# Performance work log

Hardware: AMD Instinct MI355X
Metric: run time of the kernel (lower is better)

Reference implementation:

```python
import jax, jax.numpy as jnp
import numpy as np

N, E, D, G = 50000, 640000, 128, 64
STEPS = 4

def _leaky(z):
    return jnp.where(z >= 0, z, 0.01 * z)

def _lin(x, W, b):
    return x @ W.T + b

def setup_inputs() -> dict:
    key = jax.random.key(0)
    ks = jax.random.split(key, 16)
    s = 0.05
    inp = {
        "x": jax.random.normal(ks[0], (N, D), jnp.float32),
        "x_global": jax.random.normal(ks[1], (G, D), jnp.float32),
        "edge_attr": jax.random.normal(ks[2], (E, 2), jnp.float32),
        # per-step stacked parameters (torch Linear layout [out,in])
        "Wm": jax.random.normal(ks[3], (STEPS, D, D), jnp.float32) * s,
        "bm": jnp.zeros((STEPS, D), jnp.float32),
        "Wa": jax.random.normal(ks[4], (STEPS, D, 2 * D), jnp.float32) * s,
        "ba": jnp.zeros((STEPS, D), jnp.float32),
        "Wgate": jax.random.normal(ks[5], (STEPS, 1, D), jnp.float32) * s,
        "bgate": jnp.zeros((STEPS, 1), jnp.float32),
        "Wfeat": jax.random.normal(ks[6], (STEPS, D, D), jnp.float32) * s,
        "bfeat": jnp.zeros((STEPS, D), jnp.float32),
        "Wt": jax.random.normal(ks[7], (STEPS, D, 2 * D), jnp.float32) * s,
        "bt": jnp.zeros((STEPS, D), jnp.float32),
        "edge_index": jax.random.randint(ks[8], (2, E), 0, N, jnp.int32),
        "batch_ind": jnp.sort(jax.random.randint(ks[9], (N,), 0, G, jnp.int32)),
        "num_graphs": G,
    }
    return inp

def reference(x, x_global, edge_attr, Wm, bm, Wa, ba, Wgate, bgate, Wfeat, bfeat, Wt, bt, edge_index, batch_ind, num_graphs):
    src, dst = edge_index[0], edge_index[1]
    n = x.shape[0]
    for i in range(Wm.shape[0]):
        # GraphNet: gather -> Linear+LeakyReLU -> scatter-max -> concat -> Linear+LeakyReLU + residual
        msg = _leaky(_lin(x[src], Wm[i], bm[i]))                     # [E, agg]
        agg = jax.ops.segment_max(msg, dst, num_segments=n)
        agg = jnp.where(jnp.isfinite(agg), agg, 0.0)                 # PyG fills empty with 0
        x = _leaky(_lin(jnp.concatenate([x, agg], axis=1), Wa[i], ba[i])) + x
        # GlobalNode: attentional aggregation (segment softmax) + transform + residual
        gate = _lin(x, Wgate[i], bgate[i])[:, 0]                     # [N]
        feat = _leaky(_lin(x, Wfeat[i], bfeat[i]))                   # [N, D]
        gmax = jax.ops.segment_max(gate, batch_ind, num_segments=num_graphs)
        gmax = jnp.where(jnp.isfinite(gmax), gmax, 0.0)
        e = jnp.exp(gate - gmax[batch_ind])
        denom = jax.ops.segment_sum(e, batch_ind, num_segments=num_graphs)
        denom = jnp.where(denom == 0, 1.0, denom)
        alpha = e / denom[batch_ind]
        xg = jax.ops.segment_sum(alpha[:, None] * feat, batch_ind, num_segments=num_graphs)
        cat = jnp.concatenate([xg, x_global], axis=1)
        x_global = _leaky(_lin(cat, Wt[i], bt[i])) + x_global
    return (x, x_global)
```

## Files before the change

### kernel.cpp

```cpp
#include <hip/hip_runtime.h>
#include <hip/hip_bf16.h>

#define NN 50000
#define EE 640000
#define DD 128
#define GG 64
#define STEPS 4
#define XP 32
#define NB 196

static inline int cdiv(int a, int b) { return (a + b - 1) / b; }

typedef __attribute__((ext_vector_type(8))) short bf16x8;
typedef __attribute__((ext_vector_type(4))) float f32x4;

__device__ __forceinline__ float lk(float z) { return z >= 0.f ? z : 0.01f * z; }
__device__ __forceinline__ float b2f(short b) { return __uint_as_float(((unsigned)(unsigned short)b) << 16); }
__device__ __forceinline__ unsigned short f2b(float f) {
    unsigned u = __float_as_uint(f);
    return (unsigned short)((u + 0x7FFFu + ((u >> 16) & 1u)) >> 16);
}

__global__ void k_f2b(const float* __restrict__ in, unsigned short* __restrict__ out, int n4) {
    int i = blockIdx.x * blockDim.x + threadIdx.x;
    if (i < n4) {
        float4 v = reinterpret_cast<const float4*>(in)[i];
        ushort4 o;
        o.x = f2b(v.x); o.y = f2b(v.y); o.z = f2b(v.z); o.w = f2b(v.w);
        reinterpret_cast<ushort4*>(out)[i] = o;
    }
}

#define WC1 (STEPS * DD * DD / 4)
#define WC2 (STEPS * DD * 2 * DD / 4)
#define WC3 (STEPS * DD * DD / 4)
__global__ void k_wcvt(const float* __restrict__ Wm, const float* __restrict__ Wa, const float* __restrict__ Wf,
                       unsigned short* __restrict__ Wm_b, unsigned short* __restrict__ Wa_b,
                       unsigned short* __restrict__ Wf_b) {
    int i = blockIdx.x * blockDim.x + threadIdx.x;
    const float* src; unsigned short* dst; int j = i;
    if (j < WC1) { src = Wm; dst = Wm_b; }
    else {
        j -= WC1;
        if (j < WC2) { src = Wa; dst = Wa_b; }
        else {
            j -= WC2;
            if (j >= WC3) return;
            src = Wf; dst = Wf_b;
        }
    }
    float4 v = reinterpret_cast<const float4*>(src)[j];
    ushort4 o;
    o.x = f2b(v.x); o.y = f2b(v.y); o.z = f2b(v.z); o.w = f2b(v.w);
    reinterpret_cast<ushort4*>(dst)[j] = o;
}

__global__ void k_count(const int* __restrict__ dst, int* __restrict__ deg) {
    int e = blockIdx.x * blockDim.x + threadIdx.x;
    if (e < EE) atomicAdd(&deg[dst[e]], 1);
}

__global__ __launch_bounds__(256) void k_scan1(const int* __restrict__ deg, int* __restrict__ off,
                                               int* __restrict__ bsum) {
    __shared__ int ws[4];
    int tid = threadIdx.x, lane = tid & 63, wv = tid >> 6;
    int i = blockIdx.x * 256 + tid;
    int v = (i < NN) ? deg[i] : 0;
    int x = v;
    #pragma unroll
    for (int o = 1; o < 64; o <<= 1) { int t = __shfl_up(x, o); if (lane >= o) x += t; }
    if (lane == 63) ws[wv] = x;
    __syncthreads();
    int wbase = 0;
    #pragma unroll
    for (int p = 0; p < 3; ++p) if (p < wv) wbase += ws[p];
    if (i < NN) off[i] = wbase + x - v;
    if (tid == 255) bsum[blockIdx.x] = wbase + x;
}

__global__ __launch_bounds__(256) void k_scan2(const int* __restrict__ bsum, int* __restrict__ boff,
                                               int* __restrict__ off) {
    __shared__ int ws[4];
    int tid = threadIdx.x, lane = tid & 63, wv = tid >> 6;
    int v = (tid < NB) ? bsum[tid] : 0;
    int x = v;
    #pragma unroll
    for (int o = 1; o < 64; o <<= 1) { int t = __shfl_up(x, o); if (lane >= o) x += t; }
    if (lane == 63) ws[wv] = x;
    __syncthreads();
    int wbase = 0;
    #pragma unroll
    for (int p = 0; p < 3; ++p) if (p < wv) wbase += ws[p];
    if (tid < NB) boff[tid] = wbase + x - v;
    if (tid == 255) off[NN] = wbase + x;
}

__global__ __launch_bounds__(256) void k_scan3(const int* __restrict__ boff, int* __restrict__ off,
                                               int* __restrict__ cursor) {
    int i = blockIdx.x * 256 + threadIdx.x;
    if (i < NN) {
        int o = off[i] + boff[blockIdx.x];
        off[i] = o;
        cursor[i] = o;
    }
}

__global__ void k_fill(const int* __restrict__ src, const int* __restrict__ dst,
                       int* __restrict__ cursor, int* __restrict__ csr) {
    int e = blockIdx.x * blockDim.x + threadIdx.x;
    if (e < EE) {
        int d = dst[e];
        int p = atomicAdd(&cursor[d], 1);
        csr[p] = src[e];
    }
}

__global__ void k_goff(const int* __restrict__ batch, int* __restrict__ goff) {
    int i = blockIdx.x * blockDim.x + threadIdx.x;
    if (i >= NN) return;
    int b = batch[i];
    int prev = (i == 0) ? -1 : batch[i - 1];
    for (int g = prev + 1; g <= b; ++g) goff[g] = i;
    if (i == NN - 1) for (int g = b + 1; g <= GG; ++g) goff[g] = NN;
}

template<int KDIM, bool TWO_IN, bool RESID, bool GATE, bool OUT2>
__global__ __launch_bounds__(256) void k_mfma(
    const unsigned short* __restrict__ X1b, const unsigned short* __restrict__ X2b,
    const unsigned short* __restrict__ W1, const float* __restrict__ b1,
    const unsigned short* __restrict__ W2, const float* __restrict__ b2,
    unsigned short* __restrict__ Yb1, unsigned short* __restrict__ Yb2,
    float* __restrict__ Yf, const float* __restrict__ resid,
    const float* __restrict__ wgf, const float* __restrict__ bgp, float* __restrict__ efac)
{
    __shared__ float sY[32 * 128];
    const int tid = threadIdx.x;
    const int wv = tid >> 6, lane = tid & 63;
    const int lo = lane & 15, hi = lane >> 4;
    const int rw = wv >> 1, cw = wv & 1;
    const int n0 = blockIdx.x * 32;
    const int arow = n0 + rw * 16 + lo;
    const bool rvalid = arow < NN;

    constexpr int KCH = KDIM / 32;

    bf16x8 a[KCH];
    #pragma unroll
    for (int kc = 0; kc < KCH; ++kc) {
        const int k = kc * 32 + hi * 8;
        if (rvalid) {
            if (TWO_IN) {
                const unsigned short* base = (kc < 4) ? &X1b[(size_t)arow * 128 + k]
                                                      : &X2b[(size_t)arow * 128 + (k - 128)];
                a[kc] = *reinterpret_cast<const bf16x8*>(base);
            } else {
                a[kc] = *reinterpret_cast<const bf16x8*>(&X1b[(size_t)arow * KDIM + k]);
            }
        } else {
            a[kc] = (bf16x8)(short)0;
        }
    }

    f32x4 acc1[4], acc2[4];
    #pragma unroll
    for (int t = 0; t < 4; ++t) { acc1[t] = (f32x4){0.f,0.f,0.f,0.f}; acc2[t] = (f32x4){0.f,0.f,0.f,0.f}; }

    #pragma unroll
    for (int kc = 0; kc < KCH; ++kc) {
        const int k = kc * 32 + hi * 8;
        #pragma unroll
        for (int t = 0; t < 4; ++t) {
            const int o = cw * 64 + t * 16 + lo;
            bf16x8 bv = *reinterpret_cast<const bf16x8*>(&W1[(size_t)o * KDIM + k]);
            acc1[t] = __builtin_amdgcn_mfma_f32_16x16x32_bf16(a[kc], bv, acc1[t], 0, 0, 0);
            if (OUT2) {
                bf16x8 bv2 = *reinterpret_cast<const bf16x8*>(&W2[(size_t)o * KDIM + k]);
                acc2[t] = __builtin_amdgcn_mfma_f32_16x16x32_bf16(a[kc], bv2, acc2[t], 0, 0, 0);
            }
        }
    }

    const int lrow = rw * 16 + hi * 4;
    const int swz = (hi & 1) << 4;
    #pragma unroll
    for (int t = 0; t < 4; ++t) {
        const int oc = cw * 64 + t * 16 + lo;
        const int col = oc ^ swz;
        const float bc = b1[oc];
        #pragma unroll
        for (int r = 0; r < 4; ++r)
            sY[(lrow + r) * 128 + col] = lk(acc1[t][r] + bc);
    }
    __syncthreads();

    if (RESID) {
        const float bg0 = GATE ? bgp[0] : 0.f;
        #pragma unroll
        for (int it = 0; it < 4; ++it) {
            const int idx = it * 256 + tid;
            const int row = idx >> 5, u4 = (idx & 31) * 4;
            const int n = n0 + row;
            const bool valid = n < NN;
            const int ux = u4 ^ (((row >> 2) & 1) << 4);
            float4 v = *reinterpret_cast<const float4*>(&sY[row * 128 + ux]);
            if (valid) {
                float4 rsd = *reinterpret_cast<const float4*>(&resid[(size_t)n * 128 + u4]);
                v.x += rsd.x; v.y += rsd.y; v.z += rsd.z; v.w += rsd.w;
                *reinterpret_cast<float4*>(&Yf[(size_t)n * 128 + u4]) = v;
                ushort4 ob;
                ob.x = f2b(v.x); ob.y = f2b(v.y); ob.z = f2b(v.z); ob.w = f2b(v.w);
                *reinterpret_cast<ushort4*>(&Yb1[(size_t)n * 128 + u4]) = ob;
            }
            if (GATE) {
                float4 wg4 = *reinterpret_cast<const float4*>(&wgf[u4]);
                float gs = valid ? (v.x * wg4.x + v.y * wg4.y + v.z * wg4.z + v.w * wg4.w) : 0.f;
                #pragma unroll
                for (int sh = 16; sh > 0; sh >>= 1) gs += __shfl_xor(gs, sh);
                if ((lane & 31) == 0 && valid) efac[n] = __expf(gs + bg0);
            }
        }
    } else {
        #pragma unroll
        for (int it = 0; it < 2; ++it) {
            const int idx = it * 256 + tid;
            const int row = idx >> 4, ub = (idx & 15) * 8;
            const int n = n0 + row;
            if (n < NN) {
                const int ubx = ub ^ (((row >> 2) & 1) << 4);
                bf16x8 ob;
                #pragma unroll
                for (int j = 0; j < 8; ++j) ob[j] = (short)f2b(sY[row * 128 + ubx + j]);
                *reinterpret_cast<bf16x8*>(&Yb1[(size_t)n * 128 + ub]) = ob;
            }
        }
    }

    if (OUT2) {
        __syncthreads();
        #pragma unroll
        for (int t = 0; t < 4; ++t) {
            const int oc = cw * 64 + t * 16 + lo;
            const int col = oc ^ swz;
            const float bc = b2[oc];
            #pragma unroll
            for (int r = 0; r < 4; ++r)
                sY[(lrow + r) * 128 + col] = lk(acc2[t][r] + bc);
        }
        __syncthreads();
        #pragma unroll
        for (int it = 0; it < 2; ++it) {
            const int idx = it * 256 + tid;
            const int row = idx >> 4, ub = (idx & 15) * 8;
            const int n = n0 + row;
            if (n < NN) {
                const int ubx = ub ^ (((row >> 2) & 1) << 4);
                bf16x8 ob;
                #pragma unroll
                for (int j = 0; j < 8; ++j) ob[j] = (short)f2b(sY[row * 128 + ubx + j]);
                *reinterpret_cast<bf16x8*>(&Yb2[(size_t)n * 128 + ub]) = ob;
            }
        }
    }
}

__global__ __launch_bounds__(256) void k_aggmax(const unsigned short* __restrict__ yb,
                                                const int* __restrict__ off,
                                                const int* __restrict__ csr,
                                                unsigned short* __restrict__ aggb) {
    int gtid = blockIdx.x * blockDim.x + threadIdx.x;
    int node = gtid >> 6;
    if (node >= NN) return;
    int lane = threadIdx.x & 63;
    int slot = lane >> 4, c8 = (lane & 15) * 8;
    int b = off[node], e = off[node + 1];
    int deg = e - b;
    float m[8];
    #pragma unroll
    for (int j = 0; j < 8; ++j) m[j] = -3.4e38f;
    if (deg > 0) {
        int T = (deg + 7) >> 3;
        for (int it = 0; it < T; ++it) {
            int p0 = b + it * 8 + slot;
            int p1 = p0 + 4;
            int i0 = csr[p0 < e ? p0 : b];
            int i1 = csr[p1 < e ? p1 : b];
            bf16x8 v0 = *reinterpret_cast<const bf16x8*>(&yb[(size_t)i0 * 128 + c8]);
            bf16x8 v1 = *reinterpret_cast<const bf16x8*>(&yb[(size_t)i1 * 128 + c8]);
            #pragma unroll
            for (int j = 0; j < 8; ++j) m[j] = fmaxf(m[j], fmaxf(b2f(v0[j]), b2f(v1[j])));
        }
    }
    #pragma unroll
    for (int j = 0; j < 8; ++j) m[j] = fmaxf(m[j], __shfl_xor(m[j], 16));
    #pragma unroll
    for (int j = 0; j < 8; ++j) m[j] = fmaxf(m[j], __shfl_xor(m[j], 32));
    if (slot == 0) {
        bf16x8 o;
        #pragma unroll
        for (int j = 0; j < 8; ++j) o[j] = (deg > 0) ? (short)f2b(m[j]) : (short)0;
        *reinterpret_cast<bf16x8*>(&aggb[(size_t)node * 128 + c8]) = o;
    }
}

__global__ __launch_bounds__(128) void k_xgpart(const float* __restrict__ efac,
                                                const unsigned short* __restrict__ featb,
                                                const int* __restrict__ goff,
                                                float* __restrict__ part, float* __restrict__ parte) {
    int g = blockIdx.x >> 5, p = blockIdx.x & 31;
    int d = threadIdx.x;
    int b = goff[g], e = goff[g + 1];
    int len = e - b;
    int chunk = (len + XP - 1) / XP;
    int s0 = b + p * chunk;
    int s1 = min(e, s0 + chunk);
    float acc = 0.f, acce = 0.f;
    #pragma unroll 2
    for (int i = s0; i < s1; ++i) {
        float ev = efac[i];
        acce += ev;
        acc += ev * b2f(featb[(size_t)i * 128 + d]);
    }
    part[((size_t)g * XP + p) * 128 + d] = acc;
    if (d == 0) parte[(size_t)g * XP + p] = acce;
}

__global__ __launch_bounds__(128) void k_gtrans(const float* __restrict__ part, const float* __restrict__ parte,
                                                const float* __restrict__ Wt, const float* __restrict__ bt,
                                                float* __restrict__ xglob) {
    __shared__ float cat[256];
    int g = blockIdx.x;
    int o = threadIdx.x;
    float xgv = 0.f, se = 0.f;
    #pragma unroll
    for (int p = 0; p < XP; ++p) {
        xgv += part[((size_t)g * XP + p) * 128 + o];
        se  += parte[(size_t)g * XP + p];
    }
    if (se == 0.f) se = 1.f;
    cat[o] = xgv / se;
    cat[128 + o] = xglob[(size_t)g * 128 + o];
    __syncthreads();
    float accv = bt[o];
    const float4* w4 = reinterpret_cast<const float4*>(&Wt[(size_t)o * 256]);
    #pragma unroll 8
    for (int k4 = 0; k4 < 64; ++k4) {
        float4 wv = w4[k4];
        accv += cat[4 * k4 + 0] * wv.x + cat[4 * k4 + 1] * wv.y + cat[4 * k4 + 2] * wv.z + cat[4 * k4 + 3] * wv.w;
    }
    float outv = lk(accv) + cat[128 + o];
    xglob[(size_t)g * 128 + o] = outv;
}

extern "C" void kernel_launch(void* const* d_in, const int* in_sizes, int n_in,
                              void* d_out, int out_size, void* d_ws, size_t ws_size,
                              hipStream_t stream) {
    const float* x_in  = (const float*)d_in[0];
    const float* xg_in = (const float*)d_in[1];
    const float* Wm = (const float*)d_in[3];
    const float* bm = (const float*)d_in[4];
    const float* Wa = (const float*)d_in[5];
    const float* ba = (const float*)d_in[6];
    const float* Wg = (const float*)d_in[7];
    const float* bg = (const float*)d_in[8];
    const float* Wf = (const float*)d_in[9];
    const float* bf = (const float*)d_in[10];
    const float* Wt = (const float*)d_in[11];
    const float* bt = (const float*)d_in[12];
    const int* eidx  = (const int*)d_in[13];
    const int* batch = (const int*)d_in[14];

    float* xout  = (float*)d_out;
    float* xglob = xout + (size_t)NN * DD;

    char* w = (char*)d_ws;
    unsigned short* yb    = (unsigned short*)w; w += (size_t)NN * DD * 2;
    unsigned short* featb = (unsigned short*)w; w += (size_t)NN * DD * 2;
    unsigned short* aggb  = (unsigned short*)w; w += (size_t)NN * DD * 2;
    unsigned short* xb    = (unsigned short*)w; w += (size_t)NN * DD * 2;
    unsigned short* Wm_b  = (unsigned short*)w; w += (size_t)STEPS * DD * DD * 2;
    unsigned short* Wa_b  = (unsigned short*)w; w += (size_t)STEPS * DD * 2 * DD * 2;
    unsigned short* Wf_b  = (unsigned short*)w; w += (size_t)STEPS * DD * DD * 2;
    float* efac   = (float*)w; w += (size_t)NN * 4;
    float* part   = (float*)w; w += (size_t)GG * XP * DD * 4;
    float* parte  = (float*)w; w += (size_t)GG * XP * 4;
    int* deg    = (int*)w; w += (size_t)(NN + 1) * 4;
    int* off    = (int*)w; w += (size_t)(NN + 1) * 4;
    int* cursor = (int*)w; w += (size_t)NN * 4;
    int* csr    = (int*)w; w += (size_t)EE * 4;
    int* goff   = (int*)w; w += (size_t)(GG + 1) * 4;
    int* bsum   = (int*)w; w += (size_t)NB * 4;
    int* boff   = (int*)w; w += (size_t)NB * 4;

    const int* srcI = eidx;
    const int* dstI = eidx + EE;

    hipMemcpyAsync(xout,  x_in,  (size_t)NN * DD * 4, hipMemcpyDeviceToDevice, stream);
    hipMemcpyAsync(xglob, xg_in, (size_t)GG * DD * 4, hipMemcpyDeviceToDevice, stream);

    k_f2b<<<cdiv(NN * DD / 4, 256), 256, 0, stream>>>(x_in, xb, NN * DD / 4);
    k_wcvt<<<cdiv(WC1 + WC2 + WC3, 256), 256, 0, stream>>>(Wm, Wa, Wf, Wm_b, Wa_b, Wf_b);

    hipMemsetAsync(deg, 0, (size_t)NN * 4, stream);
    k_count<<<cdiv(EE, 256), 256, 0, stream>>>(dstI, deg);
    k_scan1<<<NB, 256, 0, stream>>>(deg, off, bsum);
    k_scan2<<<1, 256, 0, stream>>>(bsum, boff, off);
    k_scan3<<<NB, 256, 0, stream>>>(boff, off, cursor);
    k_fill<<<cdiv(EE, 256), 256, 0, stream>>>(srcI, dstI, cursor, csr);
    k_goff<<<cdiv(NN, 256), 256, 0, stream>>>(batch, goff);

    const int gemmGrid = cdiv(NN, 32);
    const int aggGrid  = cdiv(NN * 64, 256);

    k_mfma<128, false, false, false, false><<<gemmGrid, 256, 0, stream>>>(
        xb, nullptr, Wm_b, bm, nullptr, nullptr, yb, nullptr, nullptr, nullptr, nullptr, nullptr, nullptr);

    for (int i = 0; i < STEPS; ++i) {
        const float* bai = ba + (size_t)i * DD;
        const unsigned short* Wai = Wa_b + (size_t)i * DD * 2 * DD;
        const float* Wgi = Wg + (size_t)i * DD;
        const float* bgi = bg + (size_t)i;
        const unsigned short* Wfi = Wf_b + (size_t)i * DD * DD;
        const float* bfi = bf + (size_t)i * DD;
        const float* Wti = Wt + (size_t)i * DD * 2 * DD;
        const float* bti = bt + (size_t)i * DD;

        k_aggmax<<<aggGrid, 256, 0, stream>>>(yb, off, csr, aggb);
        k_mfma<256, true, true, true, false><<<gemmGrid, 256, 0, stream>>>(
            xb, aggb, Wai, bai, nullptr, nullptr, xb, nullptr, xout, xout, Wgi, bgi, efac);
        if (i < STEPS - 1) {
            const unsigned short* Wmn = Wm_b + (size_t)(i + 1) * DD * DD;
            const float* bmn = bm + (size_t)(i + 1) * DD;
            k_mfma<128, false, false, false, true><<<gemmGrid, 256, 0, stream>>>(
                xb, nullptr, Wfi, bfi, Wmn, bmn, featb, yb, nullptr, nullptr, nullptr, nullptr, nullptr);
        } else {
            k_mfma<128, false, false, false, false><<<gemmGrid, 256, 0, stream>>>(
                xb, nullptr, Wfi, bfi, nullptr, nullptr, featb, nullptr, nullptr, nullptr, nullptr, nullptr, nullptr);
        }
        k_xgpart<<<GG * XP, 128, 0, stream>>>(efac, featb, goff, part, parte);
        k_gtrans<<<GG, 128, 0, stream>>>(part, parte, Wti, bti, xglob);
    }
}
```

Measured before the change: 556.2 us.

## Fuse aggregation GEMM with feature/message GEMMs into one kernel per step

Merges the Wa GEMM (with residual, gate and exp) and the following Wfeat/Wm GEMMs into a single kernel. The updated bf16 x tile stays in shared memory and feeds the second GEMM directly, so the x re-read and one launch per step go away. It also drops the initial fp32 copy of x by reading the residual from x_in on step 0, and doubles the graph-partition count in the global pooling kernel with deeper unrolling. The trade-off is more shared memory and registers per block, which may lower occupancy.

```diff
diff --git a/kernel.cpp b/kernel.cpp
--- a/kernel.cpp
+++ b/kernel.cpp
@@ -6,7 +6,7 @@
 #define DD 128
 #define GG 64
 #define STEPS 4
-#define XP 32
+#define XP 64
 #define NB 196
 
 static inline int cdiv(int a, int b) { return (a + b - 1) / b; }
@@ -124,14 +124,9 @@
     if (i == NN - 1) for (int g = b + 1; g <= GG; ++g) goff[g] = NN;
 }
 
-template<int KDIM, bool TWO_IN, bool RESID, bool GATE, bool OUT2>
-__global__ __launch_bounds__(256) void k_mfma(
-    const unsigned short* __restrict__ X1b, const unsigned short* __restrict__ X2b,
-    const unsigned short* __restrict__ W1, const float* __restrict__ b1,
-    const unsigned short* __restrict__ W2, const float* __restrict__ b2,
-    unsigned short* __restrict__ Yb1, unsigned short* __restrict__ Yb2,
-    float* __restrict__ Yf, const float* __restrict__ resid,
-    const float* __restrict__ wgf, const float* __restrict__ bgp, float* __restrict__ efac)
+__global__ __launch_bounds__(256) void k_g128(
+    const unsigned short* __restrict__ Xb, const unsigned short* __restrict__ W1,
+    const float* __restrict__ b1, unsigned short* __restrict__ Yb1)
 {
     __shared__ float sY[32 * 128];
     const int tid = threadIdx.x;
@@ -142,44 +137,25 @@
     const int arow = n0 + rw * 16 + lo;
     const bool rvalid = arow < NN;
 
-    constexpr int KCH = KDIM / 32;
-
-    bf16x8 a[KCH];
-    #pragma unroll
-    for (int kc = 0; kc < KCH; ++kc) {
+    bf16x8 a[4];
+    #pragma unroll
+    for (int kc = 0; kc < 4; ++kc) {
         const int k = kc * 32 + hi * 8;
-        if (rvalid) {
-            if (TWO_IN) {
-                const unsigned short* base = (kc < 4) ? &X1b[(size_t)arow * 128 + k]
-                                                      : &X2b[(size_t)arow * 128 + (k - 128)];
-                a[kc] = *reinterpret_cast<const bf16x8*>(base);
-            } else {
-                a[kc] = *reinterpret_cast<const bf16x8*>(&X1b[(size_t)arow * KDIM + k]);
-            }
-        } else {
-            a[kc] = (bf16x8)(short)0;
-        }
-    }
-
-    f32x4 acc1[4], acc2[4];
-    #pragma unroll
-    for (int t = 0; t < 4; ++t) { acc1[t] = (f32x4){0.f,0.f,0.f,0.f}; acc2[t] = (f32x4){0.f,0.f,0.f,0.f}; }
-
-    #pragma unroll
-    for (int kc = 0; kc < KCH; ++kc) {
+        a[kc] = rvalid ? *reinterpret_cast<const bf16x8*>(&Xb[(size_t)arow * 128 + k]) : (bf16x8)(short)0;
+    }
+    f32x4 acc[4];
+    #pragma unroll
+    for (int t = 0; t < 4; ++t) acc[t] = (f32x4){0.f,0.f,0.f,0.f};
+    #pragma unroll
+    for (int kc = 0; kc < 4; ++kc) {
         const int k = kc * 32 + hi * 8;
         #pragma unroll
         for (int t = 0; t < 4; ++t) {
             const int o = cw * 64 + t * 16 + lo;
-            bf16x8 bv = *reinterpret_cast<const bf16x8*>(&W1[(size_t)o * KDIM + k]);
-            acc1[t] = __builtin_amdgcn_mfma_f32_16x16x32_bf16(a[kc], bv, acc1[t], 0, 0, 0);
-            if (OUT2) {
-                bf16x8 bv2 = *reinterpret_cast<const bf16x8*>(&W2[(size_t)o * KDIM + k]);
-                acc2[t] = __builtin_amdgcn_mfma_f32_16x16x32_bf16(a[kc], bv2, acc2[t], 0, 0, 0);
-            }
-        }
-    }
-
+            bf16x8 bv = *reinterpret_cast<const bf16x8*>(&W1[(size_t)o * 128 + k]);
+            acc[t] = __builtin_amdgcn_mfma_f32_16x16x32_bf16(a[kc], bv, acc[t], 0, 0, 0);
+        }
+    }
     const int lrow = rw * 16 + hi * 4;
     const int swz = (hi & 1) << 4;
     #pragma unroll
@@ -188,13 +164,85 @@
         const int col = oc ^ swz;
         const float bc = b1[oc];
         #pragma unroll
-        for (int r = 0; r < 4; ++r)
-            sY[(lrow + r) * 128 + col] = lk(acc1[t][r] + bc);
-    }
-    __syncthreads();
-
-    if (RESID) {
-        const float bg0 = GATE ? bgp[0] : 0.f;
+        for (int r = 0; r < 4; ++r) sY[(lrow + r) * 128 + col] = lk(acc[t][r] + bc);
+    }
+    __syncthreads();
+    #pragma unroll
+    for (int it = 0; it < 2; ++it) {
+        const int idx = it * 256 + tid;
+        const int row = idx >> 4, ub = (idx & 15) * 8;
+        const int n = n0 + row;
+        if (n < NN) {
+            const int ubx = ub ^ (((row >> 2) & 1) << 4);
+            bf16x8 ob;
+            #pragma unroll
+            for (int j = 0; j < 8; ++j) ob[j] = (short)f2b(sY[row * 128 + ubx + j]);
+            *reinterpret_cast<bf16x8*>(&Yb1[(size_t)n * 128 + ub]) = ob;
+        }
+    }
+}
+
+template<bool MSG>
+__global__ __launch_bounds__(256) void k_mega(
+    const unsigned short* __restrict__ Xb, const unsigned short* __restrict__ Ab,
+    const unsigned short* __restrict__ Wa, const float* __restrict__ ba,
+    const float* __restrict__ resid,
+    const float* __restrict__ wgf, const float* __restrict__ bgp,
+    const unsigned short* __restrict__ Wf, const float* __restrict__ bfp,
+    const unsigned short* __restrict__ Wm2, const float* __restrict__ bm2,
+    float* __restrict__ Yf, unsigned short* __restrict__ Xbout,
+    float* __restrict__ efac, unsigned short* __restrict__ featb,
+    unsigned short* __restrict__ ybm)
+{
+    __shared__ float sY[32 * 128];
+    __shared__ unsigned short sXn[32 * 136];
+    const int tid = threadIdx.x;
+    const int wv = tid >> 6, lane = tid & 63;
+    const int lo = lane & 15, hi = lane >> 4;
+    const int rw = wv >> 1, cw = wv & 1;
+    const int n0 = blockIdx.x * 32;
+    const int arow = n0 + rw * 16 + lo;
+    const bool rvalid = arow < NN;
+
+    bf16x8 a[8];
+    #pragma unroll
+    for (int kc = 0; kc < 8; ++kc) {
+        const int k = kc * 32 + hi * 8;
+        if (rvalid) {
+            const unsigned short* base = (kc < 4) ? &Xb[(size_t)arow * 128 + k]
+                                                  : &Ab[(size_t)arow * 128 + (k - 128)];
+            a[kc] = *reinterpret_cast<const bf16x8*>(base);
+        } else a[kc] = (bf16x8)(short)0;
+    }
+
+    f32x4 acc1[4];
+    #pragma unroll
+    for (int t = 0; t < 4; ++t) acc1[t] = (f32x4){0.f,0.f,0.f,0.f};
+    #pragma unroll
+    for (int kc = 0; kc < 8; ++kc) {
+        const int k = kc * 32 + hi * 8;
+        #pragma unroll
+        for (int t = 0; t < 4; ++t) {
+            const int o = cw * 64 + t * 16 + lo;
+            bf16x8 bv = *reinterpret_cast<const bf16x8*>(&Wa[(size_t)o * 256 + k]);
+            acc1[t] = __builtin_amdgcn_mfma_f32_16x16x32_bf16(a[kc], bv, acc1[t], 0, 0, 0);
+        }
+    }
+
+    const int lrow = rw * 16 + hi * 4;
+    const int swz = (hi & 1) << 4;
+    #pragma unroll
+    for (int t = 0; t < 4; ++t) {
+        const int oc = cw * 64 + t * 16 + lo;
+        const int col = oc ^ swz;
+        const float bc = ba[oc];
+        #pragma unroll
+        for (int r = 0; r < 4; ++r) sY[(lrow + r) * 128 + col] = lk(acc1[t][r] + bc);
+    }
+    __syncthreads();
+
+    {
+        const float bg0 = bgp[0];
         #pragma unroll
         for (int it = 0; it < 4; ++it) {
             const int idx = it * 256 + tid;
@@ -207,19 +255,79 @@
                 float4 rsd = *reinterpret_cast<const float4*>(&resid[(size_t)n * 128 + u4]);
                 v.x += rsd.x; v.y += rsd.y; v.z += rsd.z; v.w += rsd.w;
                 *reinterpret_cast<float4*>(&Yf[(size_t)n * 128 + u4]) = v;
-                ushort4 ob;
-                ob.x = f2b(v.x); ob.y = f2b(v.y); ob.z = f2b(v.z); ob.w = f2b(v.w);
-                *reinterpret_cast<ushort4*>(&Yb1[(size_t)n * 128 + u4]) = ob;
             }
-            if (GATE) {
-                float4 wg4 = *reinterpret_cast<const float4*>(&wgf[u4]);
-                float gs = valid ? (v.x * wg4.x + v.y * wg4.y + v.z * wg4.z + v.w * wg4.w) : 0.f;
-                #pragma unroll
-                for (int sh = 16; sh > 0; sh >>= 1) gs += __shfl_xor(gs, sh);
-                if ((lane & 31) == 0 && valid) efac[n] = __expf(gs + bg0);
+            ushort4 ob;
+            ob.x = f2b(v.x); ob.y = f2b(v.y); ob.z = f2b(v.z); ob.w = f2b(v.w);
+            if (valid) *reinterpret_cast<ushort4*>(&Xbout[(size_t)n * 128 + u4]) = ob;
+            *reinterpret_cast<ushort4*>(&sXn[row * 136 + u4]) = ob;
+            float4 wg4 = *reinterpret_cast<const float4*>(&wgf[u4]);
+            float gs = valid ? (v.x * wg4.x + v.y * wg4.y + v.z * wg4.z + v.w * wg4.w) : 0.f;
+            #pragma unroll
+            for (int sh = 16; sh > 0; sh >>= 1) gs += __shfl_xor(gs, sh);
+            if ((lane & 31) == 0 && valid) efac[n] = __expf(gs + bg0);
+        }
+    }
+    __syncthreads();
+
+    bf16x8 a2[4];
+    #pragma unroll
+    for (int kc = 0; kc < 4; ++kc) {
+        const int k = kc * 32 + hi * 8;
+        a2[kc] = *reinterpret_cast<const bf16x8*>(&sXn[(rw * 16 + lo) * 136 + k]);
+    }
+    f32x4 accF[4], accM[4];
+    #pragma unroll
+    for (int t = 0; t < 4; ++t) { accF[t] = (f32x4){0.f,0.f,0.f,0.f}; accM[t] = (f32x4){0.f,0.f,0.f,0.f}; }
+    #pragma unroll
+    for (int kc = 0; kc < 4; ++kc) {
+        const int k = kc * 32 + hi * 8;
+        #pragma unroll
+        for (int t = 0; t < 4; ++t) {
+            const int o = cw * 64 + t * 16 + lo;
+            bf16x8 bv = *reinterpret_cast<const bf16x8*>(&Wf[(size_t)o * 128 + k]);
+            accF[t] = __builtin_amdgcn_mfma_f32_16x16x32_bf16(a2[kc], bv, accF[t], 0, 0, 0);
+            if (MSG) {
+                bf16x8 bv2 = *reinterpret_cast<const bf16x8*>(&Wm2[(size_t)o * 128 + k]);
+                accM[t] = __builtin_amdgcn_mfma_f32_16x16x32_bf16(a2[kc], bv2, accM[t], 0, 0, 0);
             }
         }
-    } else {
+    }
+    __syncthreads();
+
+    #pragma unroll
+    for (int t = 0; t < 4; ++t) {
+        const int oc = cw * 64 + t * 16 + lo;
+        const int col = oc ^ swz;
+        const float bc = bfp[oc];
+        #pragma unroll
+        for (int r = 0; r < 4; ++r) sY[(lrow + r) * 128 + col] = lk(accF[t][r] + bc);
+    }
+    __syncthreads();
+    #pragma unroll
+    for (int it = 0; it < 2; ++it) {
+        const int idx = it * 256 + tid;
+        const int row = idx >> 4, ub = (idx & 15) * 8;
+        const int n = n0 + row;
+        if (n < NN) {
+            const int ubx = ub ^ (((row >> 2) & 1) << 4);
+            bf16x8 ob;
+            #pragma unroll
+            for (int j = 0; j < 8; ++j) ob[j] = (short)f2b(sY[row * 128 + ubx + j]);
+            *reinterpret_cast<bf16x8*>(&featb[(size_t)n * 128 + ub]) = ob;
+        }
+    }
+
+    if (MSG) {
+        __syncthreads();
+        #pragma unroll
+        for (int t = 0; t < 4; ++t) {
+            const int oc = cw * 64 + t * 16 + lo;
+            const int col = oc ^ swz;
+            const float bc = bm2[oc];
+            #pragma unroll
+            for (int r = 0; r < 4; ++r) sY[(lrow + r) * 128 + col] = lk(accM[t][r] + bc);
+        }
+        __syncthreads();
         #pragma unroll
         for (int it = 0; it < 2; ++it) {
             const int idx = it * 256 + tid;
@@ -230,34 +338,7 @@
                 bf16x8 ob;
                 #pragma unroll
                 for (int j = 0; j < 8; ++j) ob[j] = (short)f2b(sY[row * 128 + ubx + j]);
-                *reinterpret_cast<bf16x8*>(&Yb1[(size_t)n * 128 + ub]) = ob;
-            }
-        }
-    }
-
-    if (OUT2) {
-        __syncthreads();
-        #pragma unroll
-        for (int t = 0; t < 4; ++t) {
-            const int oc = cw * 64 + t * 16 + lo;
-            const int col = oc ^ swz;
-            const float bc = b2[oc];
-            #pragma unroll
-            for (int r = 0; r < 4; ++r)
-                sY[(lrow + r) * 128 + col] = lk(acc2[t][r] + bc);
-        }
-        __syncthreads();
-        #pragma unroll
-        for (int it = 0; it < 2; ++it) {
-            const int idx = it * 256 + tid;
-            const int row = idx >> 4, ub = (idx & 15) * 8;
-            const int n = n0 + row;
-            if (n < NN) {
-                const int ubx = ub ^ (((row >> 2) & 1) << 4);
-                bf16x8 ob;
-                #pragma unroll
-                for (int j = 0; j < 8; ++j) ob[j] = (short)f2b(sY[row * 128 + ubx + j]);
-                *reinterpret_cast<bf16x8*>(&Yb2[(size_t)n * 128 + ub]) = ob;
+                *reinterpret_cast<bf16x8*>(&ybm[(size_t)n * 128 + ub]) = ob;
             }
         }
     }
@@ -306,7 +387,7 @@
                                                 const unsigned short* __restrict__ featb,
                                                 const int* __restrict__ goff,
                                                 float* __restrict__ part, float* __restrict__ parte) {
-    int g = blockIdx.x >> 5, p = blockIdx.x & 31;
+    int g = blockIdx.x >> 6, p = blockIdx.x & 63;
     int d = threadIdx.x;
     int b = goff[g], e = goff[g + 1];
     int len = e - b;
@@ -314,7 +395,7 @@
     int s0 = b + p * chunk;
     int s1 = min(e, s0 + chunk);
     float acc = 0.f, acce = 0.f;
-    #pragma unroll 2
+    #pragma unroll 4
     for (int i = s0; i < s1; ++i) {
         float ev = efac[i];
         acce += ev;
@@ -394,7 +475,6 @@
     const int* srcI = eidx;
     const int* dstI = eidx + EE;
 
-    hipMemcpyAsync(xout,  x_in,  (size_t)NN * DD * 4, hipMemcpyDeviceToDevice, stream);
     hipMemcpyAsync(xglob, xg_in, (size_t)GG * DD * 4, hipMemcpyDeviceToDevice, stream);
 
     k_f2b<<<cdiv(NN * DD / 4, 256), 256, 0, stream>>>(x_in, xb, NN * DD / 4);
@@ -411,8 +491,7 @@
     const int gemmGrid = cdiv(NN, 32);
     const int aggGrid  = cdiv(NN * 64, 256);
 
-    k_mfma<128, false, false, false, false><<<gemmGrid, 256, 0, stream>>>(
-        xb, nullptr, Wm_b, bm, nullptr, nullptr, yb, nullptr, nullptr, nullptr, nullptr, nullptr, nullptr);
+    k_g128<<<gemmGrid, 256, 0, stream>>>(xb, Wm_b, bm, yb);
 
     for (int i = 0; i < STEPS; ++i) {
         const float* bai = ba + (size_t)i * DD;
@@ -423,18 +502,19 @@
         const float* bfi = bf + (size_t)i * DD;
         const float* Wti = Wt + (size_t)i * DD * 2 * DD;
         const float* bti = bt + (size_t)i * DD;
+        const float* residp = (i == 0) ? x_in : xout;
 
         k_aggmax<<<aggGrid, 256, 0, stream>>>(yb, off, csr, aggb);
-        k_mfma<256, true, true, true, false><<<gemmGrid, 256, 0, stream>>>(
-            xb, aggb, Wai, bai, nullptr, nullptr, xb, nullptr, xout, xout, Wgi, bgi, efac);
         if (i < STEPS - 1) {
             const unsigned short* Wmn = Wm_b + (size_t)(i + 1) * DD * DD;
             const float* bmn = bm + (size_t)(i + 1) * DD;
-            k_mfma<128, false, false, false, true><<<gemmGrid, 256, 0, stream>>>(
-                xb, nullptr, Wfi, bfi, Wmn, bmn, featb, yb, nullptr, nullptr, nullptr, nullptr, nullptr);
+            k_mega<true><<<gemmGrid, 256, 0, stream>>>(
+                xb, aggb, Wai, bai, residp, Wgi, bgi, Wfi, bfi, Wmn, bmn,
+                xout, xb, efac, featb, yb);
         } else {
-            k_mfma<128, false, false, false, false><<<gemmGrid, 256, 0, stream>>>(
-                xb, nullptr, Wfi, bfi, nullptr, nullptr, featb, nullptr, nullptr, nullptr, nullptr, nullptr, nullptr);
+            k_mega<false><<<gemmGrid, 256, 0, stream>>>(
+                xb, aggb, Wai, bai, residp, Wgi, bgi, Wfi, bfi, nullptr, nullptr,
+                xout, xb, efac, featb, nullptr);
         }
         k_xgpart<<<GG * XP, 128, 0, stream>>>(efac, featb, goff, part, parte);
         k_gtrans<<<GG, 128, 0, stream>>>(part, parte, Wti, bti, xglob);
```

Result: faster. 529.2 us (-4.9%).
